# Kernel optimization log

Measured on AMD Instinct MI355X. Metric: run time of the kernel, lower is better.

Reference implementation:

```python
import jax, jax.numpy as jnp
import numpy as np

L1, L2, ALPHA, BETA, EPS = 0.5, 1.5, 1.0, 50000000.0, 1e-08


def tube(att, label):
    # per-row cosine/sine TUBE distance, fully vectorized over batch
    dot = jnp.sum(att * label, axis=-1)            # [B]
    p_norm = jnp.sqrt(jnp.sum(att * att, axis=-1))
    g_norm = jnp.sqrt(jnp.sum(label * label, axis=-1))
    denom = p_norm * g_norm
    cosine = jnp.where(denom == 0, 0.0, dot / jnp.where(denom == 0, 1.0, denom))
    s_s = 1.0 - jnp.square(cosine)
    # s_s < 0 -> sine = 0 ; s_s == 0 -> sqrt(s_s + eps) ; else sqrt(s_s)
    sine = jnp.where(s_s < 0, 0.0, jnp.sqrt(jnp.where(s_s <= 0, EPS, s_s)))
    r_all = p_norm * cosine / jnp.where(g_norm == 0, g_norm + EPS, g_norm)
    base = p_norm * sine + jnp.abs(g_norm - p_norm * cosine)
    ds = jnp.where(r_all >= 1, L1 * base,
         jnp.where(r_all >= 0, base,
                   L2 * jnp.abs(p_norm * cosine - g_norm - p_norm * sine)))
    ds = -jnp.log(jnp.tanh(1.0 / ds))
    return jnp.mean(ds)


def kl_loss(mu, logvar):
    return -0.5 * BETA * jnp.mean(1.0 + logvar - jnp.square(mu) - jnp.exp(logvar))


def cross_entropy(logits, label_idx):
    logp = jax.nn.log_softmax(logits, axis=-1)
    return -jnp.mean(jnp.take_along_axis(logp, label_idx[:, None], axis=1)[:, 0])


def setup_inputs() -> dict:
    key = jax.random.key(0)
    ks = jax.random.split(key, 12)
    B, C, D, Z = 16384, 100, 512, 128
    return {
        "fusion_out": jax.random.normal(ks[0], (B, C), jnp.float32),
        "comple_out": jax.random.normal(ks[1], (B, D), jnp.float32),
        "labels": jax.random.normal(ks[2], (B, C), jnp.float32),
        "labels_encoder": jax.random.normal(ks[3], (B, D), jnp.float32),
        "x_A": jax.random.normal(ks[4], (B, D), jnp.float32),
        "x_A_reconstructed": jax.random.normal(ks[5], (B, D), jnp.float32),
        "x_B": jax.random.normal(ks[6], (B, D), jnp.float32),
        "x_B_reconstructed": jax.random.normal(ks[7], (B, D), jnp.float32),
        "x_C": jax.random.normal(ks[8], (B, D), jnp.float32),
        "x_C_reconstructed": jax.random.normal(ks[9], (B, D), jnp.float32),
        "mu": jax.random.normal(ks[10], (B, Z), jnp.float32),
        "logvar": jax.random.normal(ks[11], (B, Z), jnp.float32),
    }


def reference(fusion_out, comple_out, labels, labels_encoder, x_A,
              x_A_reconstructed, x_B, x_B_reconstructed, x_C,
              x_C_reconstructed, mu, logvar):
    label_idx = jnp.argmax(labels, axis=1)
    tube_A = ALPHA * tube(x_A_reconstructed, x_A)
    tube_B = ALPHA * tube(x_B_reconstructed, x_B)
    tube_C = ALPHA * tube(x_C_reconstructed, x_C)
    kl = kl_loss(mu, logvar)
    st_all = ALPHA * tube(comple_out, labels_encoder)
    ce = cross_entropy(fusion_out, label_idx)
    return tube_A + tube_B + tube_C + kl + ce + st_all
```

## Files before the change

### kernel.cpp

```cpp
#include <hip/hip_runtime.h>
#include <math.h>

static constexpr float kL1   = 0.5f;
static constexpr float kL2   = 1.5f;
static constexpr float kBeta = 50000000.0f;
static constexpr float kEps  = 1e-08f;

__device__ __forceinline__ float waveSum(float v) {
#pragma unroll
    for (int off = 32; off > 0; off >>= 1) v += __shfl_xor(v, off, 64);
    return v;
}

__device__ __forceinline__ float tubeTail(float dot, float pp, float gg) {
    float p_norm = sqrtf(pp);
    float g_norm = sqrtf(gg);
    float denom  = p_norm * g_norm;
    float cosine = (denom == 0.0f) ? 0.0f : dot / denom;
    float s_s    = 1.0f - cosine * cosine;
    float sine   = (s_s < 0.0f) ? 0.0f : sqrtf((s_s <= 0.0f) ? kEps : s_s);
    float gd     = (g_norm == 0.0f) ? (g_norm + kEps) : g_norm;
    float pc     = p_norm * cosine;
    float r_all  = pc / gd;
    float base   = p_norm * sine + fabsf(g_norm - pc);
    float ds     = (r_all >= 1.0f) ? (kL1 * base)
                 : ((r_all >= 0.0f) ? base
                                    : kL2 * fabsf(pc - g_norm - p_norm * sine));
    float t  = 1.0f / ds;
    float em = __expf(-2.0f * t);
    return __logf(1.0f + em) - __logf(fmaxf(1.0f - em, 1e-30f));
}

#define ACC3(A, L)                                        \
    dot += A.x*L.x + A.y*L.y + A.z*L.z + A.w*L.w;         \
    pp  += A.x*A.x + A.y*A.y + A.z*A.z + A.w*A.w;         \
    gg  += L.x*L.x + L.y*L.y + L.z*L.z + L.w*L.w;

__global__ __launch_bounds__(256, 4) void fused_loss_partials(
    const float* __restrict__ fusion_out, const float* __restrict__ comple_out,
    const float* __restrict__ labels,     const float* __restrict__ labels_enc,
    const float* __restrict__ xA,  const float* __restrict__ xAr,
    const float* __restrict__ xB,  const float* __restrict__ xBr,
    const float* __restrict__ xC,  const float* __restrict__ xCr,
    const float* __restrict__ mu,  const float* __restrict__ logvar,
    float* __restrict__ partials,
    int B, int C, int Z)
{
    const int lane = threadIdx.x & 63;
    const int wave = threadIdx.x >> 6;
    const int wavesPerBlock = blockDim.x >> 6;
    const int globalWave = blockIdx.x * wavesPerBlock + wave;
    const int totalWaves = gridDim.x * wavesPerBlock;
    const int D = 512;

    float my = 0.0f;

    {
        const int h   = lane >> 5;
        const int sub = lane & 31;
        const int NP  = (4 * B) >> 1;
        const int fo  = h * 128 + sub;

        float tubeAcc = 0.0f;

        int t = globalWave;
        float4 cA0, cA1, cA2, cA3, cL0, cL1, cL2, cL3;
        if (t < NP) {
            const int row0 = 2 * t;
            const int p = row0 >> 14, r0 = row0 & (B - 1);
            const float* ab = (p == 0) ? xAr : (p == 1) ? xBr : (p == 2) ? xCr : comple_out;
            const float* lb = (p == 0) ? xA  : (p == 1) ? xB  : (p == 2) ? xC  : labels_enc;
            const float4* a = (const float4*)(ab + (size_t)r0 * D) + fo;
            const float4* l = (const float4*)(lb + (size_t)r0 * D) + fo;
            cA0 = a[0]; cA1 = a[32]; cA2 = a[64]; cA3 = a[96];
            cL0 = l[0]; cL1 = l[32]; cL2 = l[64]; cL3 = l[96];
        }
        for (; t < NP; t += totalWaves) {
            int tn = t + totalWaves;
            if (tn >= NP) tn = t;
            const int rown = 2 * tn;
            const int pn = rown >> 14, rn = rown & (B - 1);
            const float* abn = (pn == 0) ? xAr : (pn == 1) ? xBr : (pn == 2) ? xCr : comple_out;
            const float* lbn = (pn == 0) ? xA  : (pn == 1) ? xB  : (pn == 2) ? xC  : labels_enc;
            const float4* an = (const float4*)(abn + (size_t)rn * D) + fo;
            const float4* ln = (const float4*)(lbn + (size_t)rn * D) + fo;
            float4 nA0 = an[0], nA1 = an[32], nA2 = an[64], nA3 = an[96];
            float4 nL0 = ln[0], nL1 = ln[32], nL2 = ln[64], nL3 = ln[96];

            float dot = 0.0f, pp = 0.0f, gg = 0.0f;
            ACC3(cA0, cL0); ACC3(cA1, cL1); ACC3(cA2, cL2); ACC3(cA3, cL3);

#pragma unroll
            for (int off = 16; off > 0; off >>= 1) {
                dot += __shfl_xor(dot, off, 64);
                pp  += __shfl_xor(pp,  off, 64);
                gg  += __shfl_xor(gg,  off, 64);
            }

            tubeAcc += tubeTail(dot, pp, gg);

            cA0 = nA0; cA1 = nA1; cA2 = nA2; cA3 = nA3;
            cL0 = nL0; cL1 = nL1; cL2 = nL2; cL3 = nL3;
        }
        my += tubeAcc * (1.0f / (32.0f * (float)B));
    }

    {
        const int n4 = (B * Z) >> 2;
        const float4* mu4 = (const float4*)mu;
        const float4* lv4 = (const float4*)logvar;
        const int tid      = blockIdx.x * blockDim.x + threadIdx.x;
        const int nThreads = gridDim.x * blockDim.x;
        float acc = 0.0f;
        for (int i = tid; i < n4; i += nThreads) {
            float4 m = mu4[i];
            float4 l = lv4[i];
            acc += (1.0f + l.x - m.x * m.x - __expf(l.x));
            acc += (1.0f + l.y - m.y * m.y - __expf(l.y));
            acc += (1.0f + l.z - m.z * m.z - __expf(l.z));
            acc += (1.0f + l.w - m.w * m.w - __expf(l.w));
        }
        my += acc * (-0.5f * kBeta / (float)(B * Z));
    }

    {
        float acc = 0.0f;
        for (int r = globalWave; r < B; r += totalWaves) {
            const float* lrow = labels     + (size_t)r * C;
            const float* frow = fusion_out + (size_t)r * C;
            const bool has0 = (lane < C);
            const bool has1 = (lane + 64 < C);
            float v0 = has0 ? lrow[lane]      : -INFINITY;
            float v1 = has1 ? lrow[lane + 64] : -INFINITY;
            float f0 = has0 ? frow[lane]      : -INFINITY;
            float f1 = has1 ? frow[lane + 64] : -INFINITY;
            float bv; int bi;
            if (v1 > v0) { bv = v1; bi = lane + 64; } else { bv = v0; bi = lane; }
#pragma unroll
            for (int off = 32; off > 0; off >>= 1) {
                float ov = __shfl_xor(bv, off, 64);
                int   oi = __shfl_xor(bi, off, 64);
                if (ov > bv || (ov == bv && oi < bi)) { bv = ov; bi = oi; }
            }
            float m = fmaxf(f0, f1);
#pragma unroll
            for (int off = 32; off > 0; off >>= 1) m = fmaxf(m, __shfl_xor(m, off, 64));
            float e = 0.0f;
            if (has0) e += __expf(f0 - m);
            if (has1) e += __expf(f1 - m);
            e = waveSum(e);
            float tgt = (bi < 64) ? __shfl(f0, bi, 64) : __shfl(f1, bi - 64, 64);
            if (lane == 0) acc += -(tgt - m - __logf(e));
        }
        my += acc / (float)B;
    }

    float s = waveSum(my);
    __shared__ float sw[8];
    if (lane == 0) sw[wave] = s;
    __syncthreads();
    if (threadIdx.x == 0) {
        float tot = 0.0f;
        for (int i = 0; i < wavesPerBlock; ++i) tot += sw[i];
        partials[blockIdx.x] = tot;
    }
}

__global__ __launch_bounds__(256) void reduce_partials(
    const float* __restrict__ partials, float* __restrict__ out, int n)
{
    float s = 0.0f;
    for (int i = threadIdx.x; i < n; i += 256) s += partials[i];
    s = waveSum(s);
    __shared__ float sw[4];
    const int lane = threadIdx.x & 63;
    const int wave = threadIdx.x >> 6;
    if (lane == 0) sw[wave] = s;
    __syncthreads();
    if (threadIdx.x == 0) out[0] = sw[0] + sw[1] + sw[2] + sw[3];
}

extern "C" void kernel_launch(void* const* d_in, const int* in_sizes, int n_in,
                              void* d_out, int out_size, void* d_ws, size_t ws_size,
                              hipStream_t stream) {
    const float* fusion_out = (const float*)d_in[0];
    const float* comple_out = (const float*)d_in[1];
    const float* labels     = (const float*)d_in[2];
    const float* labels_enc = (const float*)d_in[3];
    const float* xA  = (const float*)d_in[4];
    const float* xAr = (const float*)d_in[5];
    const float* xB  = (const float*)d_in[6];
    const float* xBr = (const float*)d_in[7];
    const float* xC  = (const float*)d_in[8];
    const float* xCr = (const float*)d_in[9];
    const float* mu  = (const float*)d_in[10];
    const float* lv  = (const float*)d_in[11];
    float* out = (float*)d_out;
    float* ws  = (float*)d_ws;

    const int B = 16384;
    const int C = in_sizes[0] / B;
    const int Z = in_sizes[10] / B;

    const int totalBlocks = 2048;

    fused_loss_partials<<<totalBlocks, 256, 0, stream>>>(
        fusion_out, comple_out, labels, labels_enc,
        xA, xAr, xB, xBr, xC, xCr, mu, lv,
        ws, B, C, Z);
    reduce_partials<<<1, 256, 0, stream>>>(ws, out, totalBlocks);
}
```

Before: 282.6 us.

## Replace grid-stride loops with one-item-per-wave block specialization across loss terms

The persistent 2048-block grid, where every wave looped over tube pairs, KL elements and CE rows with software prefetch, is replaced by a large grid. Each block handles one kind of work: 4 wave-pairs of tube rows, 256 float4 KL elements, or 4 CE rows. This removes loop overhead and register-heavy prefetching and lets the hardware scheduler balance the work. In exchange it launches about 14k blocks, each doing a block reduction and writing a partial, so the single-block final reduce now sums about 14k partials, which may become a serial tail.

```diff
diff --git a/kernel.cpp b/kernel.cpp
--- a/kernel.cpp
+++ b/kernel.cpp
@@ -36,7 +36,7 @@
     pp  += A.x*A.x + A.y*A.y + A.z*A.z + A.w*A.w;         \
     gg  += L.x*L.x + L.y*L.y + L.z*L.z + L.w*L.w;
 
-__global__ __launch_bounds__(256, 4) void fused_loss_partials(
+__global__ __launch_bounds__(256) void fused_loss_partials(
     const float* __restrict__ fusion_out, const float* __restrict__ comple_out,
     const float* __restrict__ labels,     const float* __restrict__ labels_enc,
     const float* __restrict__ xA,  const float* __restrict__ xAr,
@@ -44,126 +44,81 @@
     const float* __restrict__ xC,  const float* __restrict__ xCr,
     const float* __restrict__ mu,  const float* __restrict__ logvar,
     float* __restrict__ partials,
-    int B, int C, int Z)
+    int C, int Z, int tubeBlocks, int klBlocks)
 {
     const int lane = threadIdx.x & 63;
     const int wave = threadIdx.x >> 6;
-    const int wavesPerBlock = blockDim.x >> 6;
-    const int globalWave = blockIdx.x * wavesPerBlock + wave;
-    const int totalWaves = gridDim.x * wavesPerBlock;
-    const int D = 512;
+    const int bid  = blockIdx.x;
+    constexpr int B = 16384;
+    constexpr int D = 512;
 
     float my = 0.0f;
 
-    {
+    if (bid < tubeBlocks) {
+        const int t   = bid * 4 + wave;
         const int h   = lane >> 5;
         const int sub = lane & 31;
-        const int NP  = (4 * B) >> 1;
-        const int fo  = h * 128 + sub;
-
-        float tubeAcc = 0.0f;
-
-        int t = globalWave;
-        float4 cA0, cA1, cA2, cA3, cL0, cL1, cL2, cL3;
-        if (t < NP) {
-            const int row0 = 2 * t;
-            const int p = row0 >> 14, r0 = row0 & (B - 1);
-            const float* ab = (p == 0) ? xAr : (p == 1) ? xBr : (p == 2) ? xCr : comple_out;
-            const float* lb = (p == 0) ? xA  : (p == 1) ? xB  : (p == 2) ? xC  : labels_enc;
-            const float4* a = (const float4*)(ab + (size_t)r0 * D) + fo;
-            const float4* l = (const float4*)(lb + (size_t)r0 * D) + fo;
-            cA0 = a[0]; cA1 = a[32]; cA2 = a[64]; cA3 = a[96];
-            cL0 = l[0]; cL1 = l[32]; cL2 = l[64]; cL3 = l[96];
+        const int p   = t >> 13;
+        const int r   = (2 * t) & (B - 1);
+        const float* ab = (p == 0) ? xAr : (p == 1) ? xBr : (p == 2) ? xCr : comple_out;
+        const float* lb = (p == 0) ? xA  : (p == 1) ? xB  : (p == 2) ? xC  : labels_enc;
+        const float4* a = (const float4*)(ab + (size_t)r * D) + (h * 128 + sub);
+        const float4* l = (const float4*)(lb + (size_t)r * D) + (h * 128 + sub);
+        float4 A0 = a[0], A1 = a[32], A2 = a[64], A3 = a[96];
+        float4 L0 = l[0], L1 = l[32], L2 = l[64], L3 = l[96];
+        float dot = 0.0f, pp = 0.0f, gg = 0.0f;
+        ACC3(A0, L0); ACC3(A1, L1); ACC3(A2, L2); ACC3(A3, L3);
+#pragma unroll
+        for (int off = 16; off > 0; off >>= 1) {
+            dot += __shfl_xor(dot, off, 64);
+            pp  += __shfl_xor(pp,  off, 64);
+            gg  += __shfl_xor(gg,  off, 64);
         }
-        for (; t < NP; t += totalWaves) {
-            int tn = t + totalWaves;
-            if (tn >= NP) tn = t;
-            const int rown = 2 * tn;
-            const int pn = rown >> 14, rn = rown & (B - 1);
-            const float* abn = (pn == 0) ? xAr : (pn == 1) ? xBr : (pn == 2) ? xCr : comple_out;
-            const float* lbn = (pn == 0) ? xA  : (pn == 1) ? xB  : (pn == 2) ? xC  : labels_enc;
-            const float4* an = (const float4*)(abn + (size_t)rn * D) + fo;
-            const float4* ln = (const float4*)(lbn + (size_t)rn * D) + fo;
-            float4 nA0 = an[0], nA1 = an[32], nA2 = an[64], nA3 = an[96];
-            float4 nL0 = ln[0], nL1 = ln[32], nL2 = ln[64], nL3 = ln[96];
-
-            float dot = 0.0f, pp = 0.0f, gg = 0.0f;
-            ACC3(cA0, cL0); ACC3(cA1, cL1); ACC3(cA2, cL2); ACC3(cA3, cL3);
-
+        my = tubeTail(dot, pp, gg) * (1.0f / (32.0f * (float)B));
+    } else if (bid < tubeBlocks + klBlocks) {
+        const int tid = (bid - tubeBlocks) * 256 + threadIdx.x;
+        const float4 m = ((const float4*)mu)[tid];
+        const float4 l = ((const float4*)logvar)[tid];
+        float acc = (1.0f + l.x - m.x * m.x - __expf(l.x))
+                  + (1.0f + l.y - m.y * m.y - __expf(l.y))
+                  + (1.0f + l.z - m.z * m.z - __expf(l.z))
+                  + (1.0f + l.w - m.w * m.w - __expf(l.w));
+        my = acc * (-0.5f * kBeta / ((float)B * (float)Z));
+    } else {
+        const int r = (bid - tubeBlocks - klBlocks) * 4 + wave;
+        const float* lrow = labels     + (size_t)r * C;
+        const float* frow = fusion_out + (size_t)r * C;
+        const bool has0 = (lane < C);
+        const bool has1 = (lane + 64 < C);
+        float v0 = has0 ? lrow[lane]      : -INFINITY;
+        float v1 = has1 ? lrow[lane + 64] : -INFINITY;
+        float f0 = has0 ? frow[lane]      : -INFINITY;
+        float f1 = has1 ? frow[lane + 64] : -INFINITY;
+        float bv; int bi;
+        if (v1 > v0) { bv = v1; bi = lane + 64; } else { bv = v0; bi = lane; }
 #pragma unroll
-            for (int off = 16; off > 0; off >>= 1) {
-                dot += __shfl_xor(dot, off, 64);
-                pp  += __shfl_xor(pp,  off, 64);
-                gg  += __shfl_xor(gg,  off, 64);
-            }
-
-            tubeAcc += tubeTail(dot, pp, gg);
-
-            cA0 = nA0; cA1 = nA1; cA2 = nA2; cA3 = nA3;
-            cL0 = nL0; cL1 = nL1; cL2 = nL2; cL3 = nL3;
+        for (int off = 32; off > 0; off >>= 1) {
+            float ov = __shfl_xor(bv, off, 64);
+            int   oi = __shfl_xor(bi, off, 64);
+            if (ov > bv || (ov == bv && oi < bi)) { bv = ov; bi = oi; }
         }
-        my += tubeAcc * (1.0f / (32.0f * (float)B));
-    }
-
-    {
-        const int n4 = (B * Z) >> 2;
-        const float4* mu4 = (const float4*)mu;
-        const float4* lv4 = (const float4*)logvar;
-        const int tid      = blockIdx.x * blockDim.x + threadIdx.x;
-        const int nThreads = gridDim.x * blockDim.x;
-        float acc = 0.0f;
-        for (int i = tid; i < n4; i += nThreads) {
-            float4 m = mu4[i];
-            float4 l = lv4[i];
-            acc += (1.0f + l.x - m.x * m.x - __expf(l.x));
-            acc += (1.0f + l.y - m.y * m.y - __expf(l.y));
-            acc += (1.0f + l.z - m.z * m.z - __expf(l.z));
-            acc += (1.0f + l.w - m.w * m.w - __expf(l.w));
-        }
-        my += acc * (-0.5f * kBeta / (float)(B * Z));
-    }
-
-    {
-        float acc = 0.0f;
-        for (int r = globalWave; r < B; r += totalWaves) {
-            const float* lrow = labels     + (size_t)r * C;
-            const float* frow = fusion_out + (size_t)r * C;
-            const bool has0 = (lane < C);
-            const bool has1 = (lane + 64 < C);
-            float v0 = has0 ? lrow[lane]      : -INFINITY;
-            float v1 = has1 ? lrow[lane + 64] : -INFINITY;
-            float f0 = has0 ? frow[lane]      : -INFINITY;
-            float f1 = has1 ? frow[lane + 64] : -INFINITY;
-            float bv; int bi;
-            if (v1 > v0) { bv = v1; bi = lane + 64; } else { bv = v0; bi = lane; }
+        float m = fmaxf(f0, f1);
 #pragma unroll
-            for (int off = 32; off > 0; off >>= 1) {
-                float ov = __shfl_xor(bv, off, 64);
-                int   oi = __shfl_xor(bi, off, 64);
-                if (ov > bv || (ov == bv && oi < bi)) { bv = ov; bi = oi; }
-            }
-            float m = fmaxf(f0, f1);
-#pragma unroll
-            for (int off = 32; off > 0; off >>= 1) m = fmaxf(m, __shfl_xor(m, off, 64));
-            float e = 0.0f;
-            if (has0) e += __expf(f0 - m);
-            if (has1) e += __expf(f1 - m);
-            e = waveSum(e);
-            float tgt = (bi < 64) ? __shfl(f0, bi, 64) : __shfl(f1, bi - 64, 64);
-            if (lane == 0) acc += -(tgt - m - __logf(e));
-        }
-        my += acc / (float)B;
+        for (int off = 32; off > 0; off >>= 1) m = fmaxf(m, __shfl_xor(m, off, 64));
+        float e = 0.0f;
+        if (has0) e += __expf(f0 - m);
+        if (has1) e += __expf(f1 - m);
+        e = waveSum(e);
+        float tgt = (bi < 64) ? __shfl(f0, bi, 64) : __shfl(f1, bi - 64, 64);
+        if (lane == 0) my = -(tgt - m - __logf(e)) / (float)B;
     }
 
     float s = waveSum(my);
-    __shared__ float sw[8];
+    __shared__ float sw[4];
     if (lane == 0) sw[wave] = s;
     __syncthreads();
-    if (threadIdx.x == 0) {
-        float tot = 0.0f;
-        for (int i = 0; i < wavesPerBlock; ++i) tot += sw[i];
-        partials[blockIdx.x] = tot;
-    }
+    if (threadIdx.x == 0)
+        partials[bid] = sw[0] + sw[1] + sw[2] + sw[3];
 }
 
 __global__ __launch_bounds__(256) void reduce_partials(
@@ -202,11 +157,14 @@
     const int C = in_sizes[0] / B;
     const int Z = in_sizes[10] / B;
 
-    const int totalBlocks = 2048;
+    const int tubeBlocks = (4 * B / 2) / 4;
+    const int klBlocks   = (B * Z / 4) / 256;
+    const int ceBlocks   = B / 4;
+    const int totalBlocks = tubeBlocks + klBlocks + ceBlocks;
 
     fused_loss_partials<<<totalBlocks, 256, 0, stream>>>(
         fusion_out, comple_out, labels, labels_enc,
         xA, xAr, xB, xBr, xC, xCr, mu, lv,
-        ws, B, C, Z);
+        ws, C, Z, tubeBlocks, klBlocks);
     reduce_partials<<<1, 256, 0, stream>>>(ws, out, totalBlocks);
 }
```

Measured after the change: 291.6 us. +3.2%, slower.
